# Kernel tuning notes

Hardware: AMD Instinct MI355X
Metric: run time of the kernel (lower is better)

The kernel has to match this reference:

```python
import jax, jax.numpy as jnp
import numpy as np
from jax import lax

B, C, V, T = 8, 256, 96, 96
C8, C2 = C // 8, C // 2


def _conv3(x, w):
    # 3x3, stride 1, pad 1, no bias (the repo's misnamed 'conv1x1')
    return lax.conv_general_dilated(x, w, (1, 1), [(1, 1), (1, 1)],
                                    dimension_numbers=("NCHW", "OIHW", "NCHW"))


def _conv1(x, w, b):
    # true 1x1 conv with bias (cAttn q/k/v)
    y = lax.conv_general_dilated(x, w, (1, 1), [(0, 0), (0, 0)],
                                 dimension_numbers=("NCHW", "OIHW", "NCHW"))
    return y + b[None, :, None, None]


def setup_inputs() -> dict:
    key = jax.random.key(0)
    ks = jax.random.split(key, 20)
    s = 0.02
    d = {
        "x": jax.random.normal(ks[0], (B, C, V, T), jnp.float32),
        # vAttn (3x3 convs, no bias)
        "v_wq": jax.random.normal(ks[1], (C8, C, 3, 3), jnp.float32) * s,
        "v_wk": jax.random.normal(ks[2], (C8, C, 3, 3), jnp.float32) * s,
        "v_wv": jax.random.normal(ks[3], (C2, C, 3, 3), jnp.float32) * s,
        "v_wo": jax.random.normal(ks[4], (C, C2, 3, 3), jnp.float32) * s,
        "v_sigma": jax.random.normal(ks[5], (1,), jnp.float32),
        # tAttn
        "t_wq": jax.random.normal(ks[6], (C8, C, 3, 3), jnp.float32) * s,
        "t_wk": jax.random.normal(ks[7], (C8, C, 3, 3), jnp.float32) * s,
        "t_wv": jax.random.normal(ks[8], (C2, C, 3, 3), jnp.float32) * s,
        "t_wo": jax.random.normal(ks[9], (C, C2, 3, 3), jnp.float32) * s,
        "t_sigma": jax.random.normal(ks[10], (1,), jnp.float32),
        # cAttn (1x1 convs with bias for q/k/v, 3x3 for output proj)
        "c_wq": jax.random.normal(ks[11], (C, C, 1, 1), jnp.float32) * s,
        "c_bq": jax.random.normal(ks[12], (C,), jnp.float32) * s,
        "c_wk": jax.random.normal(ks[13], (C, C, 1, 1), jnp.float32) * s,
        "c_bk": jax.random.normal(ks[14], (C,), jnp.float32) * s,
        "c_wv": jax.random.normal(ks[15], (C, C, 1, 1), jnp.float32) * s,
        "c_bv": jax.random.normal(ks[16], (C,), jnp.float32) * s,
        "c_wo": jax.random.normal(ks[17], (C, C, 3, 3), jnp.float32) * s,
        "c_sigma": jax.random.normal(ks[18], (1,), jnp.float32),
    }
    return d


def reference(x, v_wq, v_wk, v_wv, v_wo, v_sigma,
              t_wq, t_wk, t_wv, t_wo, t_sigma,
              c_wq, c_bq, c_wk, c_bk, c_wv, c_bv, c_wo, c_sigma):
    # vAttn: attention over the v axis, independently per (b, t)
    q = _conv3(x, v_wq)                                   # [B,C8,V,T]
    k = _conv3(x, v_wk)
    v = _conv3(x, v_wv)                                   # [B,C2,V,T]
    a = jax.nn.softmax(jnp.einsum('bcvt,bcwt->btvw', q, k), axis=-1)
    av = jnp.einsum('btvw,bcwt->bcvt', a, v)              # [B,C2,V,T]
    x1 = v_sigma * _conv3(av, v_wo)

    # tAttn: attention over the t axis, independently per (b, v)
    q = _conv3(x, t_wq)
    k = _conv3(x, t_wk)
    v = _conv3(x, t_wv)
    a = jax.nn.softmax(jnp.einsum('bcvt,bcvs->bvts', q, k), axis=-1)
    av = jnp.einsum('bvts,bcvs->bcvt', a, v)
    x2 = t_sigma * _conv3(av, t_wo)

    # cAttn: attention over the channel axis, independently per (b, v)
    q = _conv1(x, c_wq, c_bq)                             # [B,C,V,T]
    k = _conv1(x, c_wk, c_bk)
    v = _conv1(x, c_wv, c_bv)
    a = jax.nn.softmax(jnp.einsum('bcvt,bdvt->bvcd', q, k), axis=-1)
    av = jnp.einsum('bvcd,bdvt->bcvt', a, v)
    x3 = c_sigma * _conv3(av, c_wo)

    return x + x1 + x2 + x3
```

## Files before the change

### kernel.cpp

```cpp
#include <hip/hip_runtime.h>
#include <math.h>

#define BB  8
#define CH  256
#define NVT 9216
#define PLN (98*98*32)
#define PROW (98*32)

typedef short bh8 __attribute__((ext_vector_type(8)));
typedef short bh4 __attribute__((ext_vector_type(4)));
typedef float f4  __attribute__((ext_vector_type(4)));

__device__ __forceinline__ float bf2f(ushort u) {
    union { uint i; float f; } x; x.i = ((uint)u) << 16; return x.f;
}
__device__ __forceinline__ ushort f2bf(float f) {
    union { float f; uint i; } x; x.f = f;
    uint r = (x.i + 0x7FFFu + ((x.i >> 16) & 1u)) >> 16;
    return (ushort)r;
}
__device__ __forceinline__ int cperm(int ci) {
    return 8 * ((ci >> 2) & 3) + 4 * (ci >> 4) + (ci & 3);
}
__device__ __forceinline__ void gld16(const void* g, void* l) {
    __builtin_amdgcn_global_load_lds(
        (const __attribute__((address_space(1))) void*)g,
        (__attribute__((address_space(3))) void*)l, 16, 0, 0);
}

__global__ __launch_bounds__(256) void pad_zero_k(ushort* __restrict__ x32,
                                                  ushort* __restrict__ avall)
{
    int p = blockIdx.x;
    ushort* base = (p < 64) ? x32 + (size_t)p * PLN
                            : avall + (size_t)(p - 64) * PLN;
    const bh8 z = {0,0,0,0,0,0,0,0};
    for (int n = threadIdx.x; n < 1552; n += 256) {
        size_t off;
        if (n < 392)       off = (size_t)n * 8;
        else if (n < 784)  off = (size_t)97 * PROW + (size_t)(n - 392) * 8;
        else {
            int m = n - 784;
            int vq = m >> 3, side = (m >> 2) & 1, sub = m & 3;
            off = ((size_t)(vq + 1) * 98 + side * 97) * 32 + sub * 8;
        }
        *(bh8*)&base[off] = z;
    }
}

__global__ __launch_bounds__(256) void cvt_x32_k(const float* __restrict__ x,
                                                 ushort* __restrict__ x32)
{
    __shared__ ushort tile[96 * 32];
    int v = blockIdx.x, kc = blockIdx.y, b = blockIdx.z;
    int ci = threadIdx.x >> 3, tp = threadIdx.x & 7;
    const float* src = x + (((size_t)(b * 256 + kc * 32 + ci)) * 96 + v) * 96 + tp * 12;
    int pc = cperm(ci);
#pragma unroll
    for (int u = 0; u < 12; ++u)
        tile[(tp * 12 + u) * 32 + pc] = f2bf(src[u]);
    __syncthreads();
    ushort* dst = x32 + (((size_t)(b * 8 + kc) * 98 + v + 1) * 98 + 1) * 32;
    for (int n = threadIdx.x; n < 384; n += 256)
        *(bh8*)&dst[n * 8] = *(const bh8*)&tile[n * 8];
}

__global__ __launch_bounds__(256) void wpack_k(const float* __restrict__ w,
    ushort* __restrict__ dst, int CIN, int TAPS, int Csrc, int coBase, int COT,
    int kcBase, const float* __restrict__ scale)
{
    int n = blockIdx.x * 256 + threadIdx.x;
    int total = (CIN >> 5) * TAPS * Csrc * 32;
    if (n >= total) return;
    int kl  = n & 31;
    int rem = n >> 5;
    int col = rem % Csrc; rem /= Csrc;
    int tap = rem % TAPS;
    int kc  = rem / TAPS;
    int ci  = kc * 32 + kl;
    int g   = (kl >> 2) & 3;
    int i   = ((kl >> 4) << 2) | (kl & 3);
    int cog = coBase + col;
    int cot = cog >> 4, lc = cog & 15;
    float v = w[((size_t)col * CIN + ci) * TAPS + tap];
    if (scale) v *= scale[0];
    dst[((((size_t)(kcBase + kc) * TAPS + tap) * COT + cot) * 64 + (g * 16 + lc)) * 8 + i]
        = f2bf(v);
}

template<int TAPS, int CT, int OMODE>
__global__ __launch_bounds__(512, 4) void conv_mfma(
    const ushort* __restrict__ xin, const ushort* __restrict__ wpk,
    ushort* __restrict__ obf, const float* __restrict__ xres,
    float* __restrict__ oacc, const float* __restrict__ bias, int KC)
{
    constexpr int ROWS   = (TAPS == 9) ? 3 : 1;
    constexpr int SLABS  = ROWS * PROW;
    constexpr int CHUNKS = (SLABS * 2 + 1023) / 1024;
    constexpr int BUFSZ  = CHUNKS * 512;
    constexpr int COT    = CT * 4;
    constexpr int COUT   = COT * 16;
    __shared__ ushort sx[2][BUFSZ];

    const int v0 = blockIdx.x, b = blockIdx.y;
    const int tid = threadIdx.x;
    const int w = tid >> 6, l = tid & 63;
    const int g = l >> 4, lc = l & 15;
    const int wc = w & 3, wt = w >> 2;

    f4 acc[CT][3];
#pragma unroll
    for (int ct = 0; ct < CT; ++ct)
#pragma unroll
        for (int nt = 0; nt < 3; ++nt) acc[ct][nt] = (f4){0.f, 0.f, 0.f, 0.f};

    auto stage = [&](int kc, int buf) {
        const ushort* src = xin +
            (((size_t)b * KC + kc) * 98 + v0 + ((TAPS == 9) ? 0 : 1)) * (size_t)PROW;
#pragma unroll
        for (int c = 0; c < (CHUNKS + 7) / 8; ++c) {
            int ch = w + c * 8;
            if (ch < CHUNKS)
                gld16(src + ch * 512 + l * 8, &sx[buf][ch * 512 + l * 8]);
        }
    };

    stage(0, 0);
    __syncthreads();
    for (int kc = 0; kc < KC; ++kc) {
        const int cur = kc & 1;
        if (kc + 1 < KC) stage(kc + 1, cur ^ 1);
        const bh8* wp = (const bh8*)wpk;
#pragma unroll
        for (int tap = 0; tap < TAPS; ++tap) {
            const int kh = (TAPS == 9) ? tap / 3 : 0;
            const int kw = (TAPS == 9) ? tap % 3 : 1;
            bh8 af[CT];
#pragma unroll
            for (int ct = 0; ct < CT; ++ct)
                af[ct] = wp[(((size_t)kc * TAPS + tap) * COT + (wc * CT + ct)) * 64 + l];
#pragma unroll
            for (int nt = 0; nt < 3; ++nt) {
                int tp = wt * 48 + nt * 16 + lc + kw;
                bh8 bf = *(const bh8*)&sx[cur][(kh * 98 + tp) * 32 + 8 * g];
#pragma unroll
                for (int ct = 0; ct < CT; ++ct)
                    acc[ct][nt] = __builtin_amdgcn_mfma_f32_16x16x32_bf16(
                        af[ct], bf, acc[ct][nt], 0, 0, 0);
            }
        }
        __syncthreads();
    }

#pragma unroll
    for (int ct = 0; ct < CT; ++ct) {
#pragma unroll
        for (int nt = 0; nt < 3; ++nt) {
            int tt = wt * 48 + nt * 16 + lc;
            if (OMODE == 2) {
                bh4 o;
#pragma unroll
                for (int j = 0; j < 4; ++j) {
                    int cog = (wc * CT + ct) * 16 + g * 4 + j;
                    float val = acc[ct][nt][j];
                    if (bias) val += bias[cog];
                    o[j] = (short)f2bf(val);
                }
                *(bh4*)&obf[(((size_t)b * 96 + v0) * 96 + tt) * COUT
                            + (wc * CT + ct) * 16 + g * 4] = o;
            } else if (OMODE == 0) {
#pragma unroll
                for (int j = 0; j < 4; ++j) {
                    int cog = (wc * CT + ct) * 16 + g * 4 + j;
                    float val = acc[ct][nt][j];
                    if (bias) val += bias[cog];
                    obf[(((size_t)b * COUT + cog) * 96 + v0) * 96 + tt] = f2bf(val);
                }
            } else {
#pragma unroll
                for (int j = 0; j < 4; ++j) {
                    int cog = (wc * CT + ct) * 16 + g * 4 + j;
                    size_t o = (((size_t)b * COUT + cog) * 96 + v0) * 96 + tt;
                    oacc[o] = xres[o] + acc[ct][nt][j];
                }
            }
        }
    }
}

__global__ __launch_bounds__(256) void transpose_vt_k(const ushort* __restrict__ in,
                                                      ushort* __restrict__ out,
                                                      int cs_in, int cn)
{
    __shared__ ushort tile[96][100];
    int b = blockIdx.x / cn, c = blockIdx.x % cn;
    size_t sbase = ((size_t)b * cs_in + c) * NVT;
    size_t dbase = (size_t)blockIdx.x * NVT;
    for (int n = threadIdx.x; n < NVT; n += 256) tile[n / 96][n % 96] = in[sbase + n];
    __syncthreads();
    for (int n = threadIdx.x; n < NVT; n += 256) out[dbase + n] = tile[n % 96][n / 96];
}

template<bool OVER_V>
__global__ __launch_bounds__(384) void attn_vt_mfma_k(const ushort* __restrict__ qkv,
                                                      ushort* __restrict__ avall,
                                                      int sec, int cstride, int cbase)
{
    __shared__ ushort sQT[96 * 40];
    __shared__ ushort sKT[96 * 40];
    __shared__ ushort sV[128 * 104];

    int b = blockIdx.x / 96, p = blockIdx.x % 96;
    int tid = threadIdx.x;
    int wv = tid >> 6, l = tid & 63;
    int g = l >> 4, lc = l & 15;

    const size_t base = ((size_t)b * cstride + cbase) * (size_t)NVT + (size_t)p * 96;

    for (int s = tid; s < 768; s += 384) {
        int hf = s / 384;
        int c  = (s % 384) / 12;
        int m  = s % 12;
        bh8 val = *(const bh8*)&qkv[base + (size_t)(hf * 32 + c) * NVT + 8 * m];
        ushort* dst = hf ? sKT : sQT;
#pragma unroll
        for (int u = 0; u < 8; ++u)
            dst[(8 * m + u) * 40 + c] = (ushort)val[u];
    }
    for (int s = tid; s < 1536; s += 384) {
        int c = s / 12, m = s % 12;
        *(bh8*)&sV[c * 104 + 8 * m] =
            *(const bh8*)&qkv[base + (size_t)(64 + c) * NVT + 8 * m];
    }
    __syncthreads();

    bh4 qlo = *(const bh4*)&sQT[(wv * 16 + lc) * 40 + 4 * g];
    bh4 qhi = *(const bh4*)&sQT[(wv * 16 + lc) * 40 + 4 * g + 16];
    bh8 bq = __builtin_shufflevector(qlo, qhi, 0, 1, 2, 3, 4, 5, 6, 7);

    f4 st[6];
#pragma unroll
    for (int mt = 0; mt < 6; ++mt) {
        bh4 alo = *(const bh4*)&sKT[(mt * 16 + lc) * 40 + 4 * g];
        bh4 ahi = *(const bh4*)&sKT[(mt * 16 + lc) * 40 + 4 * g + 16];
        bh8 ak = __builtin_shufflevector(alo, ahi, 0, 1, 2, 3, 4, 5, 6, 7);
        st[mt] = __builtin_amdgcn_mfma_f32_16x16x32_bf16(ak, bq,
                                                         (f4){0.f, 0.f, 0.f, 0.f},
                                                         0, 0, 0);
    }

    float mx = -1e30f;
#pragma unroll
    for (int mt = 0; mt < 6; ++mt)
#pragma unroll
        for (int j = 0; j < 4; ++j) mx = fmaxf(mx, st[mt][j]);
    mx = fmaxf(mx, __shfl_xor(mx, 16));
    mx = fmaxf(mx, __shfl_xor(mx, 32));
    float sum = 0.f;
#pragma unroll
    for (int mt = 0; mt < 6; ++mt)
#pragma unroll
        for (int j = 0; j < 4; ++j) {
            float e = __expf(st[mt][j] - mx);
            st[mt][j] = e;
            sum += e;
        }
    sum += __shfl_xor(sum, 16);
    sum += __shfl_xor(sum, 32);
    float inv = 1.f / sum;

    bh8 pf[3];
#pragma unroll
    for (int ks = 0; ks < 3; ++ks) {
        bh8 t;
#pragma unroll
        for (int i = 0; i < 8; ++i)
            t[i] = (short)f2bf(st[2 * ks + (i >> 2)][i & 3] * inv);
        pf[ks] = t;
    }

    f4 acc[8];
#pragma unroll
    for (int mt = 0; mt < 8; ++mt) acc[mt] = (f4){0.f, 0.f, 0.f, 0.f};
#pragma unroll
    for (int ks = 0; ks < 3; ++ks)
#pragma unroll
        for (int mt = 0; mt < 8; ++mt) {
            bh4 alo = *(const bh4*)&sV[(mt * 16 + lc) * 104 + ks * 32 + 4 * g];
            bh4 ahi = *(const bh4*)&sV[(mt * 16 + lc) * 104 + ks * 32 + 4 * g + 16];
            bh8 avf = __builtin_shufflevector(alo, ahi, 0, 1, 2, 3, 4, 5, 6, 7);
            acc[mt] = __builtin_amdgcn_mfma_f32_16x16x32_bf16(avf, pf[ks],
                                                              acc[mt], 0, 0, 0);
        }

    int i = wv * 16 + lc;
#pragma unroll
    for (int mt = 0; mt < 8; ++mt) {
        int vv_ = OVER_V ? i : p;
        int tt_ = OVER_V ? p : i;
        bh4 o;
#pragma unroll
        for (int j = 0; j < 4; ++j) o[j] = (short)f2bf(acc[mt][j]);
        size_t off = ((((size_t)b * 16 + sec + (mt >> 1)) * 98 + 1 + vv_) * 98
                      + 1 + tt_) * 32 + 8 * g + 4 * (mt & 1);
        *(bh4*)&avall[off] = o;
    }
}

__global__ __launch_bounds__(256) void attn_c_k(const ushort* __restrict__ qc,
    const ushort* __restrict__ kc_, const ushort* __restrict__ vc,
    ushort* __restrict__ avall)
{
    __shared__ ushort sQ[64 * 104];
    __shared__ ushort sK[256 * 104];
    __shared__ ushort sV[96 * 264];
    __shared__ ushort sP[64 * 264];

    int v = blockIdx.x, cc = blockIdx.y, b = blockIdx.z;
    int c0 = cc * 64;
    int tid = threadIdx.x;
    int w = tid >> 6, l = tid & 63;
    int g = l >> 4, lc = l & 15;

    for (int s = tid; s < 64 * 12; s += 256) {
        int r = s / 12, sg = s % 12;
        *(bh8*)&sQ[r * 104 + sg * 8] =
            *(const bh8*)&qc[(((size_t)b * 256 + c0 + r) * 96 + v) * 96 + sg * 8];
    }
    for (int s = tid; s < 256 * 12; s += 256) {
        int r = s / 12, sg = s % 12;
        *(bh8*)&sK[r * 104 + sg * 8] =
            *(const bh8*)&kc_[(((size_t)b * 256 + r) * 96 + v) * 96 + sg * 8];
    }
    for (int s = tid; s < 96 * 32; s += 256) {
        int r = s / 32, sg = s % 32;
        *(bh8*)&sV[r * 264 + sg * 8] =
            *(const bh8*)&vc[(((size_t)b * 96 + v) * 96 + r) * 256 + sg * 8];
    }
    __syncthreads();

    f4 s16[16];
#pragma unroll
    for (int nt = 0; nt < 16; ++nt) s16[nt] = (f4){0.f, 0.f, 0.f, 0.f};
#pragma unroll
    for (int ks = 0; ks < 3; ++ks) {
        bh4 alo = *(const bh4*)&sQ[(w * 16 + lc) * 104 + ks * 32 + 4 * g];
        bh4 ahi = *(const bh4*)&sQ[(w * 16 + lc) * 104 + ks * 32 + 4 * g + 16];
        bh8 aq = __builtin_shufflevector(alo, ahi, 0, 1, 2, 3, 4, 5, 6, 7);
#pragma unroll
        for (int nt = 0; nt < 16; ++nt) {
            bh4 blo = *(const bh4*)&sK[(nt * 16 + lc) * 104 + ks * 32 + 4 * g];
            bh4 bhi = *(const bh4*)&sK[(nt * 16 + lc) * 104 + ks * 32 + 4 * g + 16];
            bh8 bk = __builtin_shufflevector(blo, bhi, 0, 1, 2, 3, 4, 5, 6, 7);
            s16[nt] = __builtin_amdgcn_mfma_f32_16x16x32_bf16(aq, bk, s16[nt], 0, 0, 0);
        }
    }
#pragma unroll
    for (int j = 0; j < 4; ++j) {
        float m = -1e30f;
#pragma unroll
        for (int nt = 0; nt < 16; ++nt) m = fmaxf(m, s16[nt][j]);
        m = fmaxf(m, __shfl_xor(m, 1));
        m = fmaxf(m, __shfl_xor(m, 2));
        m = fmaxf(m, __shfl_xor(m, 4));
        m = fmaxf(m, __shfl_xor(m, 8));
        float sum = 0.f;
#pragma unroll
        for (int nt = 0; nt < 16; ++nt) {
            float e = __expf(s16[nt][j] - m); s16[nt][j] = e; sum += e;
        }
        sum += __shfl_xor(sum, 1);
        sum += __shfl_xor(sum, 2);
        sum += __shfl_xor(sum, 4);
        sum += __shfl_xor(sum, 8);
        float inv = 1.f / sum;
#pragma unroll
        for (int nt = 0; nt < 16; ++nt)
            sP[(w * 16 + g * 4 + j) * 264 + nt * 16 + lc] = f2bf(s16[nt][j] * inv);
    }
    __syncthreads();

    f4 o6[6];
#pragma unroll
    for (int nt = 0; nt < 6; ++nt) o6[nt] = (f4){0.f, 0.f, 0.f, 0.f};
#pragma unroll
    for (int ks = 0; ks < 8; ++ks) {
        bh4 alo = *(const bh4*)&sP[(w * 16 + lc) * 264 + ks * 32 + 4 * g];
        bh4 ahi = *(const bh4*)&sP[(w * 16 + lc) * 264 + ks * 32 + 4 * g + 16];
        bh8 ap = __builtin_shufflevector(alo, ahi, 0, 1, 2, 3, 4, 5, 6, 7);
#pragma unroll
        for (int nt = 0; nt < 6; ++nt) {
            bh4 blo = *(const bh4*)&sV[(nt * 16 + lc) * 264 + ks * 32 + 4 * g];
            bh4 bhi = *(const bh4*)&sV[(nt * 16 + lc) * 264 + ks * 32 + 4 * g + 16];
            bh8 bv = __builtin_shufflevector(blo, bhi, 0, 1, 2, 3, 4, 5, 6, 7);
            o6[nt] = __builtin_amdgcn_mfma_f32_16x16x32_bf16(ap, bv, o6[nt], 0, 0, 0);
        }
    }
#pragma unroll
    for (int nt = 0; nt < 6; ++nt) {
        int t = nt * 16 + lc;
        bh4 o;
#pragma unroll
        for (int j = 0; j < 4; ++j) o[j] = (short)f2bf(o6[nt][j]);
        size_t off = ((((size_t)b * 16 + 8 + cc * 2 + (w >> 1)) * 98 + 1 + v) * 98
                      + 1 + t) * 32 + 8 * g + 4 * (w & 1);
        *(bh4*)&avall[off] = o;
    }
}

extern "C" void kernel_launch(void* const* d_in, const int* in_sizes, int n_in,
                              void* d_out, int out_size, void* d_ws, size_t ws_size,
                              hipStream_t stream)
{
    const float* x     = (const float*)d_in[0];
    const float* v_wq  = (const float*)d_in[1];
    const float* v_wk  = (const float*)d_in[2];
    const float* v_wv  = (const float*)d_in[3];
    const float* v_wo  = (const float*)d_in[4];
    const float* v_sig = (const float*)d_in[5];
    const float* t_wq  = (const float*)d_in[6];
    const float* t_wk  = (const float*)d_in[7];
    const float* t_wv  = (const float*)d_in[8];
    const float* t_wo  = (const float*)d_in[9];
    const float* t_sig = (const float*)d_in[10];
    const float* c_wq  = (const float*)d_in[11];
    const float* c_bq  = (const float*)d_in[12];
    const float* c_wk  = (const float*)d_in[13];
    const float* c_bk  = (const float*)d_in[14];
    const float* c_wv  = (const float*)d_in[15];
    const float* c_bv  = (const float*)d_in[16];
    const float* c_wo  = (const float*)d_in[17];
    const float* c_sig = (const float*)d_in[18];

    float*  out = (float*)d_out;
    ushort* ws  = (ushort*)d_ws;

    const size_t X32   = 0;
    const size_t AVL   = X32 + 19685376;
    const size_t POOL  = AVL + 39354368;
    const size_t QKVV  = POOL;
    const size_t QKVVT = POOL + 14155776;
    const size_t QKVT_ = POOL + 28311552;
    const size_t QC    = POOL;
    const size_t KCB   = POOL + 18874368;
    const size_t VCT   = POOL + 42467328;
    const size_t PK    = VCT + 18874368;
    const size_t PK_PV  = PK;
    const size_t PK_PT  = PK_PV + 442368;
    const size_t PK_CQ  = PK_PT + 442368;
    const size_t PK_CK  = PK_CQ + 65536;
    const size_t PK_CV  = PK_CK + 65536;
    const size_t PK_FIN = PK_CV + 65536;

    pad_zero_k<<<192, 256, 0, stream>>>(ws + X32, ws + AVL);
    cvt_x32_k<<<dim3(96, 8, BB), 256, 0, stream>>>(x, ws + X32);

    auto pack = [&](const float* w, size_t dst, int cin, int taps, int csrc,
                    int cobase, int cot, int kcb, const float* sc) {
        int total = (cin >> 5) * taps * csrc * 32;
        wpack_k<<<(total + 255) / 256, 256, 0, stream>>>(w, ws + dst, cin, taps,
                                                          csrc, cobase, cot, kcb, sc);
    };
    pack(v_wq, PK_PV, 256, 9, 32, 0, 12, 0, nullptr);
    pack(v_wk, PK_PV, 256, 9, 32, 32, 12, 0, nullptr);
    pack(v_wv, PK_PV, 256, 9, 128, 64, 12, 0, nullptr);
    pack(t_wq, PK_PT, 256, 9, 32, 0, 12, 0, nullptr);
    pack(t_wk, PK_PT, 256, 9, 32, 32, 12, 0, nullptr);
    pack(t_wv, PK_PT, 256, 9, 128, 64, 12, 0, nullptr);
    pack(c_wq, PK_CQ, 256, 1, 256, 0, 16, 0, nullptr);
    pack(c_wk, PK_CK, 256, 1, 256, 0, 16, 0, nullptr);
    pack(c_wv, PK_CV, 256, 1, 256, 0, 16, 0, nullptr);
    pack(v_wo, PK_FIN, 128, 9, 256, 0, 16, 0, v_sig);
    pack(t_wo, PK_FIN, 128, 9, 256, 0, 16, 4, t_sig);
    pack(c_wo, PK_FIN, 256, 9, 256, 0, 16, 8, c_sig);

    dim3 cgrid(96, BB);

    conv_mfma<9, 3, 0><<<cgrid, 512, 0, stream>>>(
        ws + X32, ws + PK_PV, ws + QKVV, nullptr, nullptr, nullptr, 8);
    transpose_vt_k<<<BB * 192, 256, 0, stream>>>(ws + QKVV, ws + QKVVT, 192, 192);
    attn_vt_mfma_k<true><<<BB * 96, 384, 0, stream>>>(ws + QKVVT, ws + AVL, 0, 192, 0);

    conv_mfma<9, 3, 0><<<cgrid, 512, 0, stream>>>(
        ws + X32, ws + PK_PT, ws + QKVT_, nullptr, nullptr, nullptr, 8);
    attn_vt_mfma_k<false><<<BB * 96, 384, 0, stream>>>(ws + QKVT_, ws + AVL, 4, 192, 0);

    conv_mfma<1, 4, 0><<<cgrid, 512, 0, stream>>>(
        ws + X32, ws + PK_CQ, ws + QC, nullptr, nullptr, c_bq, 8);
    conv_mfma<1, 4, 0><<<cgrid, 512, 0, stream>>>(
        ws + X32, ws + PK_CK, ws + KCB, nullptr, nullptr, c_bk, 8);
    conv_mfma<1, 4, 2><<<cgrid, 512, 0, stream>>>(
        ws + X32, ws + PK_CV, ws + VCT, nullptr, nullptr, c_bv, 8);
    attn_c_k<<<dim3(96, 4, BB), 256, 0, stream>>>(ws + QC, ws + KCB, ws + VCT,
                                                  ws + AVL);

    conv_mfma<9, 4, 5><<<cgrid, 512, 0, stream>>>(
        ws + AVL, ws + PK_FIN, nullptr, x, out, nullptr, 16);
}
```

Measured before the change: 716.9 us.

## Merge v/t and cq/ck projection convs, swizzle LDS layout, remap block order

Result: slower. 993.7 us (+38.6%).

```diff
diff --git a/kernel.cpp b/kernel.cpp
--- a/kernel.cpp
+++ b/kernel.cpp
@@ -56,9 +56,13 @@
     int ci = threadIdx.x >> 3, tp = threadIdx.x & 7;
     const float* src = x + (((size_t)(b * 256 + kc * 32 + ci)) * 96 + v) * 96 + tp * 12;
     int pc = cperm(ci);
-#pragma unroll
-    for (int u = 0; u < 12; ++u)
-        tile[(tp * 12 + u) * 32 + pc] = f2bf(src[u]);
+    int gci = pc >> 3, idx = pc & 7;
+#pragma unroll
+    for (int u = 0; u < 12; ++u) {
+        int t = tp * 12 + u;
+        int sw = ((t + 1) >> 1) & 3;
+        tile[t * 32 + 8 * (gci ^ sw) + idx] = f2bf(src[u]);
+    }
     __syncthreads();
     ushort* dst = x32 + (((size_t)(b * 8 + kc) * 98 + v + 1) * 98 + 1) * 32;
     for (int n = threadIdx.x; n < 384; n += 256)
@@ -92,7 +96,8 @@
 __global__ __launch_bounds__(512, 4) void conv_mfma(
     const ushort* __restrict__ xin, const ushort* __restrict__ wpk,
     ushort* __restrict__ obf, const float* __restrict__ xres,
-    float* __restrict__ oacc, const float* __restrict__ bias, int KC)
+    float* __restrict__ oacc, const float* __restrict__ bias,
+    const float* __restrict__ bias2, int KC)
 {
     constexpr int ROWS   = (TAPS == 9) ? 3 : 1;
     constexpr int SLABS  = ROWS * PROW;
@@ -102,7 +107,8 @@
     constexpr int COUT   = COT * 16;
     __shared__ ushort sx[2][BUFSZ];
 
-    const int v0 = blockIdx.x, b = blockIdx.y;
+    const int bx = blockIdx.x, b = blockIdx.y;
+    const int v0 = (bx & 7) * 12 + (bx >> 3);
     const int tid = threadIdx.x;
     const int w = tid >> 6, l = tid & 63;
     const int g = l >> 4, lc = l & 15;
@@ -142,7 +148,8 @@
 #pragma unroll
             for (int nt = 0; nt < 3; ++nt) {
                 int tp = wt * 48 + nt * 16 + lc + kw;
-                bh8 bf = *(const bh8*)&sx[cur][(kh * 98 + tp) * 32 + 8 * g];
+                bh8 bf = *(const bh8*)&sx[cur][(kh * 98 + tp) * 32
+                                              + 8 * (g ^ ((tp >> 1) & 3))];
 #pragma unroll
                 for (int ct = 0; ct < CT; ++ct)
                     acc[ct][nt] = __builtin_amdgcn_mfma_f32_16x16x32_bf16(
@@ -163,7 +170,7 @@
                 for (int j = 0; j < 4; ++j) {
                     int cog = (wc * CT + ct) * 16 + g * 4 + j;
                     float val = acc[ct][nt][j];
-                    if (bias) val += bias[cog];
+                    if (bias) val += (cog < 256) ? bias[cog] : bias2[cog - 256];
                     o[j] = (short)f2bf(val);
                 }
                 *(bh4*)&obf[(((size_t)b * 96 + v0) * 96 + tt) * COUT
@@ -173,7 +180,7 @@
                 for (int j = 0; j < 4; ++j) {
                     int cog = (wc * CT + ct) * 16 + g * 4 + j;
                     float val = acc[ct][nt][j];
-                    if (bias) val += bias[cog];
+                    if (bias) val += (cog < 256) ? bias[cog] : bias2[cog - 256];
                     obf[(((size_t)b * COUT + cog) * 96 + v0) * 96 + tt] = f2bf(val);
                 }
             } else {
@@ -298,18 +305,18 @@
     for (int mt = 0; mt < 8; ++mt) {
         int vv_ = OVER_V ? i : p;
         int tt_ = OVER_V ? p : i;
+        int sw  = ((1 + tt_) >> 1) & 3;
         bh4 o;
 #pragma unroll
         for (int j = 0; j < 4; ++j) o[j] = (short)f2bf(acc[mt][j]);
         size_t off = ((((size_t)b * 16 + sec + (mt >> 1)) * 98 + 1 + vv_) * 98
-                      + 1 + tt_) * 32 + 8 * g + 4 * (mt & 1);
+                      + 1 + tt_) * 32 + 8 * (g ^ sw) + 4 * (mt & 1);
         *(bh4*)&avall[off] = o;
     }
 }
 
-__global__ __launch_bounds__(256) void attn_c_k(const ushort* __restrict__ qc,
-    const ushort* __restrict__ kc_, const ushort* __restrict__ vc,
-    ushort* __restrict__ avall)
+__global__ __launch_bounds__(256) void attn_c_k(const ushort* __restrict__ qkc,
+    const ushort* __restrict__ vc, ushort* __restrict__ avall)
 {
     __shared__ ushort sQ[64 * 104];
     __shared__ ushort sK[256 * 104];
@@ -325,12 +332,12 @@
     for (int s = tid; s < 64 * 12; s += 256) {
         int r = s / 12, sg = s % 12;
         *(bh8*)&sQ[r * 104 + sg * 8] =
-            *(const bh8*)&qc[(((size_t)b * 256 + c0 + r) * 96 + v) * 96 + sg * 8];
+            *(const bh8*)&qkc[(((size_t)b * 512 + c0 + r) * 96 + v) * 96 + sg * 8];
     }
     for (int s = tid; s < 256 * 12; s += 256) {
         int r = s / 12, sg = s % 12;
         *(bh8*)&sK[r * 104 + sg * 8] =
-            *(const bh8*)&kc_[(((size_t)b * 256 + r) * 96 + v) * 96 + sg * 8];
+            *(const bh8*)&qkc[(((size_t)b * 512 + 256 + r) * 96 + v) * 96 + sg * 8];
     }
     for (int s = tid; s < 96 * 32; s += 256) {
         int r = s / 32, sg = s % 32;
@@ -399,11 +406,12 @@
 #pragma unroll
     for (int nt = 0; nt < 6; ++nt) {
         int t = nt * 16 + lc;
+        int sw = ((1 + t) >> 1) & 3;
         bh4 o;
 #pragma unroll
         for (int j = 0; j < 4; ++j) o[j] = (short)f2bf(o6[nt][j]);
         size_t off = ((((size_t)b * 16 + 8 + cc * 2 + (w >> 1)) * 98 + 1 + v) * 98
-                      + 1 + t) * 32 + 8 * g + 4 * (w & 1);
+                      + 1 + t) * 32 + 8 * (g ^ sw) + 4 * (w & 1);
         *(bh4*)&avall[off] = o;
     }
 }
@@ -435,21 +443,17 @@
     float*  out = (float*)d_out;
     ushort* ws  = (ushort*)d_ws;
 
-    const size_t X32   = 0;
-    const size_t AVL   = X32 + 19685376;
-    const size_t POOL  = AVL + 39354368;
-    const size_t QKVV  = POOL;
-    const size_t QKVVT = POOL + 14155776;
-    const size_t QKVT_ = POOL + 28311552;
-    const size_t QC    = POOL;
-    const size_t KCB   = POOL + 18874368;
-    const size_t VCT   = POOL + 42467328;
-    const size_t PK    = VCT + 18874368;
-    const size_t PK_PV  = PK;
-    const size_t PK_PT  = PK_PV + 442368;
-    const size_t PK_CQ  = PK_PT + 442368;
-    const size_t PK_CK  = PK_CQ + 65536;
-    const size_t PK_CV  = PK_CK + 65536;
+    const size_t X32  = 0;
+    const size_t AVL  = X32 + 19685376;
+    const size_t POOL = AVL + 39354368;
+    const size_t QKV   = POOL;
+    const size_t QKVVT = POOL + 28311552;
+    const size_t QKC   = POOL;
+    const size_t VCT   = POOL + 37748736;
+    const size_t PK    = POOL + 56623104;
+    const size_t PK_PVT = PK;
+    const size_t PK_CQK = PK_PVT + 884736;
+    const size_t PK_CV  = PK_CQK + 131072;
     const size_t PK_FIN = PK_CV + 65536;
 
     pad_zero_k<<<192, 256, 0, stream>>>(ws + X32, ws + AVL);
@@ -461,14 +465,14 @@
         wpack_k<<<(total + 255) / 256, 256, 0, stream>>>(w, ws + dst, cin, taps,
                                                           csrc, cobase, cot, kcb, sc);
     };
-    pack(v_wq, PK_PV, 256, 9, 32, 0, 12, 0, nullptr);
-    pack(v_wk, PK_PV, 256, 9, 32, 32, 12, 0, nullptr);
-    pack(v_wv, PK_PV, 256, 9, 128, 64, 12, 0, nullptr);
-    pack(t_wq, PK_PT, 256, 9, 32, 0, 12, 0, nullptr);
-    pack(t_wk, PK_PT, 256, 9, 32, 32, 12, 0, nullptr);
-    pack(t_wv, PK_PT, 256, 9, 128, 64, 12, 0, nullptr);
-    pack(c_wq, PK_CQ, 256, 1, 256, 0, 16, 0, nullptr);
-    pack(c_wk, PK_CK, 256, 1, 256, 0, 16, 0, nullptr);
+    pack(v_wq, PK_PVT, 256, 9, 32, 0, 24, 0, nullptr);
+    pack(v_wk, PK_PVT, 256, 9, 32, 32, 24, 0, nullptr);
+    pack(v_wv, PK_PVT, 256, 9, 128, 64, 24, 0, nullptr);
+    pack(t_wq, PK_PVT, 256, 9, 32, 192, 24, 0, nullptr);
+    pack(t_wk, PK_PVT, 256, 9, 32, 224, 24, 0, nullptr);
+    pack(t_wv, PK_PVT, 256, 9, 128, 256, 24, 0, nullptr);
+    pack(c_wq, PK_CQK, 256, 1, 256, 0, 32, 0, nullptr);
+    pack(c_wk, PK_CQK, 256, 1, 256, 256, 32, 0, nullptr);
     pack(c_wv, PK_CV, 256, 1, 256, 0, 16, 0, nullptr);
     pack(v_wo, PK_FIN, 128, 9, 256, 0, 16, 0, v_sig);
     pack(t_wo, PK_FIN, 128, 9, 256, 0, 16, 4, t_sig);
@@ -476,24 +480,20 @@
 
     dim3 cgrid(96, BB);
 
-    conv_mfma<9, 3, 0><<<cgrid, 512, 0, stream>>>(
-        ws + X32, ws + PK_PV, ws + QKVV, nullptr, nullptr, nullptr, 8);
-    transpose_vt_k<<<BB * 192, 256, 0, stream>>>(ws + QKVV, ws + QKVVT, 192, 192);
+    conv_mfma<9, 6, 0><<<cgrid, 512, 0, stream>>>(
+        ws + X32, ws + PK_PVT, ws + QKV, nullptr, nullptr, nullptr, nullptr, 8);
+
+    transpose_vt_k<<<BB * 192, 256, 0, stream>>>(ws + QKV, ws + QKVVT, 384, 192);
     attn_vt_mfma_k<true><<<BB * 96, 384, 0, stream>>>(ws + QKVVT, ws + AVL, 0, 192, 0);
 
-    conv_mfma<9, 3, 0><<<cgrid, 512, 0, stream>>>(
-        ws + X32, ws + PK_PT, ws + QKVT_, nullptr, nullptr, nullptr, 8);
-    attn_vt_mfma_k<false><<<BB * 96, 384, 0, stream>>>(ws + QKVT_, ws + AVL, 4, 192, 0);
-
-    conv_mfma<1, 4, 0><<<cgrid, 512, 0, stream>>>(
-        ws + X32, ws + PK_CQ, ws + QC, nullptr, nullptr, c_bq, 8);
-    conv_mfma<1, 4, 0><<<cgrid, 512, 0, stream>>>(
-        ws + X32, ws + PK_CK, ws + KCB, nullptr, nullptr, c_bk, 8);
+    attn_vt_mfma_k<false><<<BB * 96, 384, 0, stream>>>(ws + QKV, ws + AVL, 4, 384, 192);
+
+    conv_mfma<1, 8, 0><<<cgrid, 512, 0, stream>>>(
+        ws + X32, ws + PK_CQK, ws + QKC, nullptr, nullptr, c_bq, c_bk, 8);
     conv_mfma<1, 4, 2><<<cgrid, 512, 0, stream>>>(
-        ws + X32, ws + PK_CV, ws + VCT, nullptr, nullptr, c_bv, 8);
-    attn_c_k<<<dim3(96, 4, BB), 256, 0, stream>>>(ws + QC, ws + KCB, ws + VCT,
-                                                  ws + AVL);
+        ws + X32, ws + PK_CV, ws + VCT, nullptr, nullptr, c_bv, nullptr, 8);
+    attn_c_k<<<dim3(96, 4, BB), 256, 0, stream>>>(ws + QKC, ws + VCT, ws + AVL);
 
     conv_mfma<9, 4, 5><<<cgrid, 512, 0, stream>>>(
-        ws + AVL, ws + PK_FIN, nullptr, x, out, nullptr, 16);
-}
+        ws + AVL, ws + PK_FIN, nullptr, x, out, nullptr, nullptr, 16);
+}
```
